# Performance work log

Hardware: AMD Instinct MI355X
Metric: run time of the kernel (lower is better)

## Reference

```python
import jax, jax.numpy as jnp
import numpy as np

N_ENT = 100000   # n_entities
N_REL = 40       # n_relations_ckg
D = 64           # embed_dim
L = 3            # n_layers
E = 1000000      # number of CKG triples (edges)


def setup_inputs() -> dict:
    key = jax.random.key(0)
    k = jax.random.split(key, 6)
    xavier = np.sqrt(6.0 / (D + D))  # xavier_uniform for square Linear
    return {
        "heads": jax.random.randint(k[0], (E,), 0, N_ENT),
        "rels": jax.random.randint(k[1], (E,), 0, N_REL),
        "tails": jax.random.randint(k[2], (E,), 0, N_ENT),
        "entity_embed": 0.01 * jax.random.normal(k[3], (N_ENT, D), dtype=jnp.float32),
        "rel_embeds": 0.01 * jax.random.normal(k[4], (L, N_REL, D), dtype=jnp.float32),
        "Ws": (jax.random.uniform(k[5], (L, D, D), minval=-1.0, maxval=1.0) * xavier).astype(jnp.float32),
    }


def _kgat_layer(h, heads, rels, tails, rel_emb, W):
    # h: [N, D]; heads/rels/tails: [E]; rel_emb: [n_rel, D]; W: [D, D] (nn.Linear weight)
    n = h.shape[0]
    e_h = h[heads]            # [E, D] gather
    e_t = h[tails]            # [E, D] gather
    e_r = rel_emb[rels]       # [E, D] gather
    # pi(h,r,t) = e_t . tanh(e_h + e_r)
    score = jnp.sum(e_t * jnp.tanh(e_h + e_r), axis=-1)          # [E]
    score = score - jax.lax.stop_gradient(jnp.max(score))        # global shift (detach)
    score_exp = jnp.exp(score)                                   # [E]
    score_sum = jax.ops.segment_sum(score_exp, heads, num_segments=n)  # [N]
    attn = score_exp / (score_sum[heads] + 1e-10)                # [E] per-head softmax
    agg = jax.ops.segment_sum(attn[:, None] * e_t, heads, num_segments=n)  # [N, D]
    out = (h + agg) @ W.T                                        # Linear, no bias
    return jax.nn.leaky_relu(out, negative_slope=0.2)            # dropout = identity (eval)


def reference(heads, rels, tails, entity_embed, rel_embeds, Ws):
    h = entity_embed
    all_layers = [h]
    for l in range(rel_embeds.shape[0]):
        h = _kgat_layer(h, heads, rels, tails, rel_embeds[l], Ws[l])
        all_layers.append(h)
    return jnp.concatenate(all_layers, axis=-1)  # [N, D*(L+1)]
```

## Files before the change

kernel.cpp:

```cpp
#include <hip/hip_runtime.h>

#define DD 64
#define ROW 256
#define CHUNK 1024

__global__ void k_copy_count(const float* __restrict__ ent, float* __restrict__ out,
                             const int* __restrict__ heads, int* __restrict__ counts,
                             int* __restrict__ permpos, int n_rows, int nE) {
    int idx = blockIdx.x * blockDim.x + threadIdx.x;
    int total = n_rows * 16;
    if (idx < total) {
        int n = idx >> 4, q = idx & 15;
        const float4* src = (const float4*)(ent + (long)n * DD);
        float4* dst = (float4*)(out + (long)n * ROW);
        dst[q] = src[q];
    }
    if (idx < nE) {
        permpos[idx] = atomicAdd(counts + heads[idx], 1);
    }
}

__global__ __launch_bounds__(256) void k_scan_chunk(
        const int* __restrict__ counts, int* __restrict__ offs,
        int* __restrict__ partials, int n) {
    __shared__ int lds[256];
    int base = blockIdx.x * CHUNK;
    int t = threadIdx.x;
    int c[4]; int sum = 0;
    #pragma unroll
    for (int j = 0; j < 4; ++j) {
        int i = base + t * 4 + j;
        c[j] = (i < n) ? counts[i] : 0;
        sum += c[j];
    }
    lds[t] = sum; __syncthreads();
    for (int d = 1; d < 256; d <<= 1) {
        int v = (t >= d) ? lds[t - d] : 0;
        __syncthreads();
        lds[t] += v;
        __syncthreads();
    }
    int excl = lds[t] - sum;
    if (t == 255) partials[blockIdx.x] = lds[255];
    int run = excl;
    #pragma unroll
    for (int j = 0; j < 4; ++j) {
        int i = base + t * 4 + j;
        if (i < n) offs[i] = run;
        run += c[j];
    }
}

__global__ __launch_bounds__(256) void k_scan_add(
        int* __restrict__ offs, const int* __restrict__ partials,
        int n, int nE, int nchunks) {
    __shared__ int lds[128];
    int t = threadIdx.x;
    if (t < 128) {
        int v = (t < nchunks) ? partials[t] : 0;
        lds[t] = v;
    }
    __syncthreads();
    for (int d = 1; d < 128; d <<= 1) {
        int u = (t < 128 && t >= d) ? lds[t - d] : 0;
        __syncthreads();
        if (t < 128) lds[t] += u;
        __syncthreads();
    }
    int i = blockIdx.x * 256 + t;
    if (i < n) {
        int ck = i >> 10;
        int excl = (ck == 0) ? 0 : lds[ck - 1];
        offs[i] += excl;
    } else if (i == n) {
        offs[n] = nE;
    }
}

__global__ void k_scatter(const int* __restrict__ heads, const int* __restrict__ rels,
                          const int* __restrict__ tails, const int* __restrict__ offs,
                          const int* __restrict__ permpos,
                          int* __restrict__ packed, int nE) {
    int e = blockIdx.x * 256 + threadIdx.x;
    if (e >= nE) return;
    int h = heads[e];
    packed[offs[h] + permpos[e]] = tails[e] | (rels[e] << 20);
}

__global__ __launch_bounds__(256) void k_layer(
        const int* __restrict__ offs, const int* __restrict__ packed,
        const float* __restrict__ hbase, const float* __restrict__ relemb,
        const float* __restrict__ W, float* __restrict__ outbase,
        int n_heads, int nE) {
    __shared__ float Wt[DD * 65];
    __shared__ float xs[4][DD];
    for (int idx = threadIdx.x; idx < DD * DD; idx += 256)
        Wt[(idx & 63) * 65 + (idx >> 6)] = W[idx];
    __syncthreads();

    int w = threadIdx.x >> 6, lane = threadIdx.x & 63;
    int g = lane >> 4, s = lane & 15;

    for (int hd = blockIdx.x * 4 + w; hd < n_heads; hd += gridDim.x * 4) {
        const float4 eh4 = *(const float4*)(hbase + (long)hd * ROW + 4 * s);
        float4 acc = make_float4(0.f, 0.f, 0.f, 0.f);
        float ssum = 0.f;
        int p0 = offs[hd], pe = offs[hd + 1];

        for (int cbase = p0; cbase < pe; cbase += 64) {
            int clen = min(pe - cbase, 64);
            int vAll = packed[min(cbase + lane, nE - 1)];

            int i0 = (g < clen) ? g : 0;
            int i1 = (4 + g < clen) ? 4 + g : 0;
            int v0 = __shfl(vAll, i0);
            int v1 = __shfl(vAll, i1);
            float4 tt0 = *(const float4*)(hbase + (long)(v0 & 0xFFFFF) * ROW + 4 * s);
            float4 rr0 = *(const float4*)(relemb + (v0 >> 20) * DD + 4 * s);
            float4 tt1 = *(const float4*)(hbase + (long)(v1 & 0xFFFFF) * ROW + 4 * s);
            float4 rr1 = *(const float4*)(relemb + (v1 >> 20) * DD + 4 * s);

            for (int i = 0; i < clen; i += 8) {
                int ia = i + 8 + g;  ia = (ia < clen) ? ia : 0;
                int ib = i + 12 + g; ib = (ib < clen) ? ib : 0;
                int va = __shfl(vAll, ia);
                int vb = __shfl(vAll, ib);
                float4 tta = *(const float4*)(hbase + (long)(va & 0xFFFFF) * ROW + 4 * s);
                float4 rra = *(const float4*)(relemb + (va >> 20) * DD + 4 * s);
                float4 ttb = *(const float4*)(hbase + (long)(vb & 0xFFFFF) * ROW + 4 * s);
                float4 rrb = *(const float4*)(relemb + (vb >> 20) * DD + 4 * s);

                {
                    float sc = 0.f;
                    #pragma unroll
                    for (int q = 0; q < 4; ++q) {
                        float xq = (&eh4.x)[q] + (&rr0.x)[q];
                        float t = __expf(2.f * xq);
                        float th = 1.f - 2.f * __builtin_amdgcn_rcpf(t + 1.f);
                        sc += (&tt0.x)[q] * th;
                    }
                    #pragma unroll
                    for (int off = 1; off <= 8; off <<= 1) sc += __shfl_xor(sc, off);
                    float se = ((i + g) < clen) ? __expf(sc) : 0.f;
                    ssum += se;
                    acc.x += se * tt0.x; acc.y += se * tt0.y;
                    acc.z += se * tt0.z; acc.w += se * tt0.w;
                }
                {
                    float sc = 0.f;
                    #pragma unroll
                    for (int q = 0; q < 4; ++q) {
                        float xq = (&eh4.x)[q] + (&rr1.x)[q];
                        float t = __expf(2.f * xq);
                        float th = 1.f - 2.f * __builtin_amdgcn_rcpf(t + 1.f);
                        sc += (&tt1.x)[q] * th;
                    }
                    #pragma unroll
                    for (int off = 1; off <= 8; off <<= 1) sc += __shfl_xor(sc, off);
                    float se = ((i + 4 + g) < clen) ? __expf(sc) : 0.f;
                    ssum += se;
                    acc.x += se * tt1.x; acc.y += se * tt1.y;
                    acc.z += se * tt1.z; acc.w += se * tt1.w;
                }
                tt0 = tta; rr0 = rra; tt1 = ttb; rr1 = rrb;
            }
        }

        #pragma unroll
        for (int off = 16; off <= 32; off <<= 1) {
            acc.x += __shfl_xor(acc.x, off);
            acc.y += __shfl_xor(acc.y, off);
            acc.z += __shfl_xor(acc.z, off);
            acc.w += __shfl_xor(acc.w, off);
            ssum  += __shfl_xor(ssum,  off);
        }
        float inv = 1.f / (ssum + 1e-10f);
        float4 x4;
        x4.x = eh4.x + acc.x * inv;  x4.y = eh4.y + acc.y * inv;
        x4.z = eh4.z + acc.z * inv;  x4.w = eh4.w + acc.w * inv;
        if (g == 0) *(float4*)(&xs[w][4 * s]) = x4;

        float y = 0.f;
        const float* xw = xs[w];
        #pragma unroll
        for (int k4 = 0; k4 < DD; k4 += 4) {
            float4 xv = *(const float4*)(xw + k4);
            y += xv.x * Wt[(k4 + 0) * 65 + lane];
            y += xv.y * Wt[(k4 + 1) * 65 + lane];
            y += xv.z * Wt[(k4 + 2) * 65 + lane];
            y += xv.w * Wt[(k4 + 3) * 65 + lane];
        }
        y = y >= 0.f ? y : 0.2f * y;
        outbase[(long)hd * ROW + lane] = y;
    }
}

extern "C" void kernel_launch(void* const* d_in, const int* in_sizes, int n_in,
                              void* d_out, int out_size, void* d_ws, size_t ws_size,
                              hipStream_t stream) {
    const int*   heads = (const int*)d_in[0];
    const int*   rels  = (const int*)d_in[1];
    const int*   tails = (const int*)d_in[2];
    const float* ent   = (const float*)d_in[3];
    const float* rel   = (const float*)d_in[4];
    const float* Ws    = (const float*)d_in[5];
    float* out = (float*)d_out;

    const int nE = in_sizes[0];
    const int N  = in_sizes[3] / DD;
    const int L  = in_sizes[5] / (DD * DD);
    const int NREL = in_sizes[4] / (L * DD);

    int* offs    = (int*)d_ws;
    int* counts  = offs + (N + 1);
    int* packed  = counts + N;
    int* permpos = packed + nE;
    int* partials = packed + nE - 128;

    dim3 blk(256);
    int nchunks = (N + CHUNK - 1) / CHUNK;
    int fuse_total = max(N * 16, nE);

    hipMemsetAsync(counts, 0, (size_t)N * sizeof(int), stream);
    k_copy_count<<<(fuse_total + 255) / 256, blk, 0, stream>>>(ent, out, heads, counts, permpos, N, nE);
    k_scan_chunk<<<nchunks, blk, 0, stream>>>(counts, offs, partials, N);
    k_scan_add<<<(N + 1 + 255) / 256, blk, 0, stream>>>(offs, partials, N, nE, nchunks);
    k_scatter<<<(nE + 255) / 256, blk, 0, stream>>>(heads, rels, tails, offs, permpos, packed, nE);

    for (int l = 0; l < L; ++l) {
        k_layer<<<2048, blk, 0, stream>>>(
            offs, packed, out + l * DD, rel + (long)l * NREL * DD,
            Ws + (long)l * DD * DD, out + (l + 1) * DD, N, nE);
    }
}
```

Measured before the change: 454.5 us.

## Replace CSR scan/scatter with fixed-capacity per-head buckets and overflow fallback

Edges are written directly into per-head buckets of capacity 64 during the counting pass. This removes the prefix-scan kernels and the separate scatter kernel. If any head exceeds the capacity, a single-block fallback rebuilds the compact CSR layout, and the layer kernel picks the addressing mode from the overflow flag. The cost is a larger sparse buffer (N*64 ints) with strided, less coalesced bucket writes. The fallback runs as one block, which would be very slow whenever it triggers.

```diff
diff --git a/kernel.cpp b/kernel.cpp
--- a/kernel.cpp
+++ b/kernel.cpp
@@ -2,11 +2,13 @@
 
 #define DD 64
 #define ROW 256
-#define CHUNK 1024
-
-__global__ void k_copy_count(const float* __restrict__ ent, float* __restrict__ out,
-                             const int* __restrict__ heads, int* __restrict__ counts,
-                             int* __restrict__ permpos, int n_rows, int nE) {
+#define CAP 64
+
+__global__ void k_build(const float* __restrict__ ent, float* __restrict__ out,
+                        const int* __restrict__ heads, const int* __restrict__ rels,
+                        const int* __restrict__ tails, int* __restrict__ counts,
+                        int* __restrict__ ovf, int* __restrict__ permpos,
+                        int* __restrict__ packedF, int n_rows, int nE) {
     int idx = blockIdx.x * blockDim.x + threadIdx.x;
     int total = n_rows * 16;
     if (idx < total) {
@@ -16,79 +18,47 @@
         dst[q] = src[q];
     }
     if (idx < nE) {
-        permpos[idx] = atomicAdd(counts + heads[idx], 1);
-    }
-}
-
-__global__ __launch_bounds__(256) void k_scan_chunk(
-        const int* __restrict__ counts, int* __restrict__ offs,
-        int* __restrict__ partials, int n) {
-    __shared__ int lds[256];
-    int base = blockIdx.x * CHUNK;
+        int h = heads[idx];
+        int rank = atomicAdd(counts + h, 1);
+        permpos[idx] = rank;
+        if (rank < CAP) packedF[(long)h * CAP + rank] = tails[idx] | (rels[idx] << 20);
+        else *ovf = 1;
+    }
+}
+
+__global__ __launch_bounds__(1024) void k_fallback(
+        const int* __restrict__ heads, const int* __restrict__ rels,
+        const int* __restrict__ tails, const int* __restrict__ counts,
+        const int* __restrict__ ovf, int* __restrict__ offs,
+        const int* __restrict__ permpos, int* __restrict__ packed,
+        int n, int nE) {
+    if (*ovf == 0) return;
+    __shared__ int lds[1024];
     int t = threadIdx.x;
-    int c[4]; int sum = 0;
-    #pragma unroll
-    for (int j = 0; j < 4; ++j) {
-        int i = base + t * 4 + j;
-        c[j] = (i < n) ? counts[i] : 0;
-        sum += c[j];
-    }
+    int per = (n + 1023) / 1024;
+    int lo = t * per, hi = min(lo + per, n);
+    int sum = 0;
+    for (int i = lo; i < hi; ++i) sum += counts[i];
     lds[t] = sum; __syncthreads();
-    for (int d = 1; d < 256; d <<= 1) {
-        int v = (t >= d) ? lds[t - d] : 0;
+    for (int d = 1; d < 1024; d <<= 1) {
+        int u = (t >= d) ? lds[t - d] : 0;
         __syncthreads();
-        lds[t] += v;
+        lds[t] += u;
         __syncthreads();
     }
-    int excl = lds[t] - sum;
-    if (t == 255) partials[blockIdx.x] = lds[255];
-    int run = excl;
-    #pragma unroll
-    for (int j = 0; j < 4; ++j) {
-        int i = base + t * 4 + j;
-        if (i < n) offs[i] = run;
-        run += c[j];
-    }
-}
-
-__global__ __launch_bounds__(256) void k_scan_add(
-        int* __restrict__ offs, const int* __restrict__ partials,
-        int n, int nE, int nchunks) {
-    __shared__ int lds[128];
-    int t = threadIdx.x;
-    if (t < 128) {
-        int v = (t < nchunks) ? partials[t] : 0;
-        lds[t] = v;
-    }
+    int run = lds[t] - sum;
+    for (int i = lo; i < hi; ++i) { offs[i] = run; run += counts[i]; }
+    if (t == 0) offs[n] = nE;
     __syncthreads();
-    for (int d = 1; d < 128; d <<= 1) {
-        int u = (t < 128 && t >= d) ? lds[t - d] : 0;
-        __syncthreads();
-        if (t < 128) lds[t] += u;
-        __syncthreads();
-    }
-    int i = blockIdx.x * 256 + t;
-    if (i < n) {
-        int ck = i >> 10;
-        int excl = (ck == 0) ? 0 : lds[ck - 1];
-        offs[i] += excl;
-    } else if (i == n) {
-        offs[n] = nE;
-    }
-}
-
-__global__ void k_scatter(const int* __restrict__ heads, const int* __restrict__ rels,
-                          const int* __restrict__ tails, const int* __restrict__ offs,
-                          const int* __restrict__ permpos,
-                          int* __restrict__ packed, int nE) {
-    int e = blockIdx.x * 256 + threadIdx.x;
-    if (e >= nE) return;
-    int h = heads[e];
-    packed[offs[h] + permpos[e]] = tails[e] | (rels[e] << 20);
+    for (int e = t; e < nE; e += 1024) {
+        int h = heads[e];
+        packed[offs[h] + permpos[e]] = tails[e] | (rels[e] << 20);
+    }
 }
 
 __global__ __launch_bounds__(256) void k_layer(
-        const int* __restrict__ offs, const int* __restrict__ packed,
+        const int* __restrict__ offs, const int* __restrict__ counts,
+        const int* __restrict__ ovf, const int* __restrict__ packed,
         const float* __restrict__ hbase, const float* __restrict__ relemb,
         const float* __restrict__ W, float* __restrict__ outbase,
         int n_heads, int nE) {
@@ -98,6 +68,9 @@
         Wt[(idx & 63) * 65 + (idx >> 6)] = W[idx];
     __syncthreads();
 
+    const int mode = *ovf;
+    const int cap = n_heads * CAP - 1;
+
     int w = threadIdx.x >> 6, lane = threadIdx.x & 63;
     int g = lane >> 4, s = lane & 15;
 
@@ -105,11 +78,13 @@
         const float4 eh4 = *(const float4*)(hbase + (long)hd * ROW + 4 * s);
         float4 acc = make_float4(0.f, 0.f, 0.f, 0.f);
         float ssum = 0.f;
-        int p0 = offs[hd], pe = offs[hd + 1];
+        int p0, pe;
+        if (mode == 0) { p0 = hd << 6; pe = p0 + counts[hd]; }
+        else           { p0 = offs[hd]; pe = offs[hd + 1]; }
 
         for (int cbase = p0; cbase < pe; cbase += 64) {
             int clen = min(pe - cbase, 64);
-            int vAll = packed[min(cbase + lane, nE - 1)];
+            int vAll = packed[min(cbase + lane, cap)];
 
             int i0 = (g < clen) ? g : 0;
             int i1 = (4 + g < clen) ? 4 + g : 0;
@@ -211,25 +186,24 @@
     const int L  = in_sizes[5] / (DD * DD);
     const int NREL = in_sizes[4] / (L * DD);
 
-    int* offs    = (int*)d_ws;
-    int* counts  = offs + (N + 1);
-    int* packed  = counts + N;
-    int* permpos = packed + nE;
-    int* partials = packed + nE - 128;
+    int* counts  = (int*)d_ws;
+    int* ovf     = counts + N;
+    int* offs    = ovf + 1;
+    int* permpos = offs + (N + 1);
+    int* packedF = permpos + nE;
 
     dim3 blk(256);
-    int nchunks = (N + CHUNK - 1) / CHUNK;
     int fuse_total = max(N * 16, nE);
 
-    hipMemsetAsync(counts, 0, (size_t)N * sizeof(int), stream);
-    k_copy_count<<<(fuse_total + 255) / 256, blk, 0, stream>>>(ent, out, heads, counts, permpos, N, nE);
-    k_scan_chunk<<<nchunks, blk, 0, stream>>>(counts, offs, partials, N);
-    k_scan_add<<<(N + 1 + 255) / 256, blk, 0, stream>>>(offs, partials, N, nE, nchunks);
-    k_scatter<<<(nE + 255) / 256, blk, 0, stream>>>(heads, rels, tails, offs, permpos, packed, nE);
+    hipMemsetAsync(counts, 0, (size_t)(N + 1) * sizeof(int), stream);
+    k_build<<<(fuse_total + 255) / 256, blk, 0, stream>>>(
+        ent, out, heads, rels, tails, counts, ovf, permpos, packedF, N, nE);
+    k_fallback<<<1, 1024, 0, stream>>>(
+        heads, rels, tails, counts, ovf, offs, permpos, packedF, N, nE);
 
     for (int l = 0; l < L; ++l) {
         k_layer<<<2048, blk, 0, stream>>>(
-            offs, packed, out + l * DD, rel + (long)l * NREL * DD,
+            offs, counts, ovf, packedF, out + l * DD, rel + (long)l * NREL * DD,
             Ws + (long)l * DD * DD, out + (l + 1) * DD, N, nE);
     }
 }
```

Result: no change. 452.2 us (-0.5%).
